# Kernel tuning notes

Hardware: AMD Instinct MI355X
Metric: run time of the kernel (lower is better)

The kernel has to match this reference:

```python
import jax, jax.numpy as jnp
import numpy as np


def setup_inputs() -> dict:
    key = jax.random.key(0)
    ks = jax.random.split(key, 8)
    n_src, n_dst, n_edges = 100000, 50000, 600000
    d_in, d_out = 128, 128
    n_reuse, n_cache = 5000, 8000
    full_dst_len = n_dst + n_reuse

    feat_src = jax.random.normal(ks[0], (n_src, d_in), jnp.float32)
    src = jax.random.randint(ks[1], (n_edges,), 0, n_src)
    dst = jax.random.randint(ks[2], (n_edges,), 0, n_dst)
    # xavier-ish init for the two bias-free Linear layers (stored as [out, in] like torch)
    W_self = jax.random.normal(ks[3], (d_out, d_in), jnp.float32) / np.sqrt(d_in).astype(np.float32)
    W_neigh = jax.random.normal(ks[4], (d_out, d_in), jnp.float32) / np.sqrt(d_in).astype(np.float32)
    # reuse_indices must be unique positions within [0, full_dst_len)
    reuse_indices = jnp.sort(jax.random.permutation(ks[5], full_dst_len)[:n_reuse])
    reuse_embedding = jax.random.normal(ks[6], (n_reuse, d_out), jnp.float32)
    cache_indices = jax.random.randint(ks[7], (n_cache,), 0, full_dst_len)
    return dict(feat_src=feat_src, W_self=W_self, W_neigh=W_neigh,
                reuse_embedding=reuse_embedding, src=src, dst=dst,
                reuse_indices=reuse_indices, cache_indices=cache_indices,
                n_dst=n_dst)


def reference(feat_src, W_self, W_neigh, reuse_embedding, src, dst,
              reuse_indices, cache_indices, n_dst):
    # --- GraphSAGE 'mean' aggregation on a block graph ---
    feat_dst = feat_src[:n_dst]                         # [n_dst, D_in]
    msgs = feat_src[src]                                # [E, D_in] copy_src gather
    ssum = jax.ops.segment_sum(msgs, dst, num_segments=n_dst)          # [n_dst, D_in]
    deg = jax.ops.segment_sum(jnp.ones_like(msgs[:, 0]), dst, num_segments=n_dst)
    h_neigh = jnp.where(deg[:, None] > 0, ssum / jnp.maximum(deg, 1.0)[:, None], 0.0)
    rst = feat_dst @ W_self.T + h_neigh @ W_neigh.T     # fc_self + fc_neigh

    # --- cache-reuse scatter merge (flag == 0 path) ---
    n_reuse = reuse_indices.shape[0]
    full_dst_len = n_dst + n_reuse
    keep = jnp.ones((full_dst_len,), dtype=bool).at[reuse_indices].set(False)
    unprune_indices = jnp.nonzero(keep, size=n_dst)[0]  # np.delete equivalent
    full = jnp.zeros((full_dst_len, rst.shape[1]), rst.dtype)
    full = full.at[unprune_indices].set(rst).at[reuse_indices].set(reuse_embedding)
    cache_embedding = jax.lax.stop_gradient(full[cache_indices])  # .detach()
    return full, cache_embedding
```

## Files before the change

### kernel.cpp

```cpp
#include <hip/hip_runtime.h>

#define N_SRC   100000
#define N_DST   50000
#define D       128
#define MAXDEG  64

#define NB      391
#define CHUNKS  256
#define TOTAL_BLOCKS 2048
#define COUNT_BLOCKS 256

typedef __attribute__((ext_vector_type(8))) short bf16x8;
typedef __attribute__((ext_vector_type(4))) float f32x4;

__device__ __forceinline__ unsigned short f2bf(float f) {
    unsigned u = __float_as_uint(f);
    u += 0x7FFFu + ((u >> 16) & 1u);
    return (unsigned short)(u >> 16);
}
__device__ __forceinline__ float bf2f(unsigned short u) {
    return __uint_as_float((unsigned)u << 16);
}

__global__ __launch_bounds__(256)
void prep_count_kernel(const int* __restrict__ dst,
                       int* __restrict__ cntmatT,
                       int n_edges, int cb,
                       const int* __restrict__ reuse_idx,
                       int* __restrict__ rowpos, int n_reuse,
                       const float* __restrict__ Wself,
                       const float* __restrict__ Wneigh,
                       unsigned short* __restrict__ wbf,
                       const float* __restrict__ feat,
                       unsigned int* __restrict__ featbf_u32) {
    __shared__ int lc[NB];
    if (blockIdx.x < COUNT_BLOCKS) {
        for (int i = threadIdx.x; i < NB; i += 256) lc[i] = 0;
        __syncthreads();
        int c = blockIdx.x;
        int e0 = c * cb, e1 = min(n_edges, e0 + cb);
        for (int e = e0 + (int)threadIdx.x; e < e1; e += 256)
            atomicAdd(&lc[dst[e] >> 7], 1);
        __syncthreads();
        for (int i = threadIdx.x; i < NB; i += 256)
            cntmatT[i * CHUNKS + c] = lc[i];
    } else {
        int stid = (blockIdx.x - COUNT_BLOCKS) * 256 + threadIdx.x;
        const int sstride = (TOTAL_BLOCKS - COUNT_BLOCKS) * 256;

        if (stid < N_DST) {
            int lo = 0, hi = n_reuse;
            while (lo < hi) {
                int mid = (lo + hi) >> 1;
                if (reuse_idx[mid] - mid > stid) hi = mid; else lo = mid + 1;
            }
            rowpos[stid] = stid + lo;
        }
        if (stid < 128 * 256) {
            int n = stid >> 8;
            int k = stid & 255;
            float v = (k < 128) ? Wself[n * 128 + k] : Wneigh[n * 128 + (k - 128)];
            wbf[stid] = f2bf(v);
        }
        const int n4 = N_SRC * (D / 4);
        for (int i = stid; i < n4; i += sstride) {
            float4 v = *(const float4*)(feat + (size_t)i * 4);
            uint2 o;
            o.x = (unsigned)f2bf(v.x) | ((unsigned)f2bf(v.y) << 16);
            o.y = (unsigned)f2bf(v.z) | ((unsigned)f2bf(v.w) << 16);
            *(uint2*)(featbf_u32 + (size_t)i * 2) = o;
        }
    }
}

__global__ __launch_bounds__(256)
void bucket_scan_kernel(const int* __restrict__ cntmatT,
                        int* __restrict__ offrel,
                        int* __restrict__ bsum) {
    __shared__ int s[CHUNKS];
    int k = blockIdx.x;
    int t = threadIdx.x;
    int x = cntmatT[k * CHUNKS + t];
    s[t] = x;
    __syncthreads();
#pragma unroll
    for (int off = 1; off < CHUNKS; off <<= 1) {
        int v = (t >= off) ? s[t - off] : 0;
        __syncthreads();
        s[t] += v;
        __syncthreads();
    }
    offrel[k * CHUNKS + t] = s[t] - x;
    if (t == CHUNKS - 1) bsum[k] = s[t];
}

__global__ __launch_bounds__(256)
void base_scan_kernel(const int* __restrict__ bsum,
                      int* __restrict__ bucketbase) {
    __shared__ int s[NB];
    __shared__ int tot;
    int t = threadIdx.x;
    for (int i = t; i < NB; i += 256) s[i] = bsum[i];
    __syncthreads();
    if (t == 0) {
        int run = 0;
        for (int i = 0; i < NB; ++i) { int v = s[i]; s[i] = run; run += v; }
        tot = run;
    }
    __syncthreads();
    for (int i = t; i < NB; i += 256) bucketbase[i] = s[i];
    if (t == 0) bucketbase[NB] = tot;
}

__global__ __launch_bounds__(256)
void scatter_kernel(const int* __restrict__ src,
                    const int* __restrict__ dst,
                    const int* __restrict__ offrel,
                    const int* __restrict__ bucketbase,
                    uint2* __restrict__ pe,
                    int n_edges, int cb) {
    __shared__ int lc[NB];
    for (int i = threadIdx.x; i < NB; i += 256) lc[i] = 0;
    __syncthreads();
    int c = blockIdx.x;
    int e0 = c * cb, e1 = min(n_edges, e0 + cb);
    for (int e = e0 + (int)threadIdx.x; e < e1; e += 256) {
        int d = dst[e];
        int s = src[e];
        int k = d >> 7;
        int r = atomicAdd(&lc[k], 1);
        int pos = bucketbase[k] + offrel[k * CHUNKS + c] + r;
        pe[pos] = make_uint2((unsigned)s, (unsigned)d);
    }
}

__global__ __launch_bounds__(256)
void fine_ell_kernel(const uint2* __restrict__ pe,
                     const int* __restrict__ bucketbase,
                     int* __restrict__ ell,
                     int* __restrict__ cnt) {
    __shared__ int rc[128];
    int k = blockIdx.x;
    if (threadIdx.x < 128) rc[threadIdx.x] = 0;
    __syncthreads();
    int e0 = bucketbase[k], e1 = bucketbase[k + 1];
    for (int e = e0 + (int)threadIdx.x; e < e1; e += 256) {
        uint2 p = pe[e];
        int d = (int)p.y;
        int slot = atomicAdd(&rc[d & 127], 1);
        if (slot < MAXDEG)
            ell[(size_t)d * MAXDEG + slot] = (int)p.x;
    }
    __syncthreads();
    int row = k * 128 + threadIdx.x;
    if (threadIdx.x < 128 && row < N_DST) cnt[row] = rc[threadIdx.x];
}

__global__ __launch_bounds__(256)
void gather_bf16_kernel(const unsigned short* __restrict__ featbf,
                        const int* __restrict__ ell,
                        const int* __restrict__ cnt,
                        uint4* __restrict__ hneigh_u4) {
    int gid  = blockIdx.x * blockDim.x + threadIdx.x;
    int row  = gid >> 4;
    int lane = gid & 15;
    if (row >= N_DST) return;

    int deg = cnt[row];
    int n = min(deg, MAXDEG);
    float inv = 1.0f / fmaxf((float)deg, 1.0f);
    const int* rell = ell + (size_t)row * MAXDEG;

    float acc[8];
#pragma unroll
    for (int k = 0; k < 8; ++k) acc[k] = 0.f;

    union U { uint4 v; unsigned short us[8]; };
    int j = 0;
    for (; j + 4 <= n; j += 4) {
        int s0 = rell[j + 0];
        int s1 = rell[j + 1];
        int s2 = rell[j + 2];
        int s3 = rell[j + 3];
        U a, b, c, d;
        a.v = *(const uint4*)(featbf + (size_t)s0 * D + lane * 8);
        b.v = *(const uint4*)(featbf + (size_t)s1 * D + lane * 8);
        c.v = *(const uint4*)(featbf + (size_t)s2 * D + lane * 8);
        d.v = *(const uint4*)(featbf + (size_t)s3 * D + lane * 8);
#pragma unroll
        for (int k = 0; k < 8; ++k)
            acc[k] += (bf2f(a.us[k]) + bf2f(b.us[k])) + (bf2f(c.us[k]) + bf2f(d.us[k]));
    }
    for (; j < n; ++j) {
        int s = rell[j];
        U a;
        a.v = *(const uint4*)(featbf + (size_t)s * D + lane * 8);
#pragma unroll
        for (int k = 0; k < 8; ++k) acc[k] += bf2f(a.us[k]);
    }
    uint4 o;
    o.x = (unsigned)f2bf(acc[0] * inv) | ((unsigned)f2bf(acc[1] * inv) << 16);
    o.y = (unsigned)f2bf(acc[2] * inv) | ((unsigned)f2bf(acc[3] * inv) << 16);
    o.z = (unsigned)f2bf(acc[4] * inv) | ((unsigned)f2bf(acc[5] * inv) << 16);
    o.w = (unsigned)f2bf(acc[6] * inv) | ((unsigned)f2bf(acc[7] * inv) << 16);
    hneigh_u4[(size_t)row * 16 + lane] = o;
}

__global__ __launch_bounds__(256, 2)
void gemm_kernel(const unsigned short* __restrict__ featbf,
                 const unsigned short* __restrict__ hneigh,
                 const unsigned short* __restrict__ wbf,
                 const int* __restrict__ rowpos,
                 float* __restrict__ full) {
    __shared__ unsigned short Wl[128 * 256];

    int tid = threadIdx.x;
    {
        int n = tid >> 1;
        int ckbase = (tid & 1) * 16;
        const uint4* s = (const uint4*)(wbf + n * 256);
        uint4* d = (uint4*)(Wl + n * 256);
#pragma unroll
        for (int i = 0; i < 16; ++i) {
            int ck = ckbase + i;
            d[ck ^ (n & 7)] = s[ck];
        }
    }
    __syncthreads();

    int wv   = tid >> 6;
    int lane = tid & 63;
    int l15  = lane & 15;
    int q    = lane >> 4;
    int rowbase = blockIdx.x * 128 + wv * 32;

    f32x4 acc[2][8];
#pragma unroll
    for (int rt = 0; rt < 2; ++rt)
#pragma unroll
        for (int ct = 0; ct < 8; ++ct) acc[rt][ct] = (f32x4){0.f, 0.f, 0.f, 0.f};

    int r0c = min(rowbase + l15,      N_DST - 1);
    int r1c = min(rowbase + 16 + l15, N_DST - 1);

#pragma unroll
    for (int s = 0; s < 8; ++s) {
        const unsigned short* A = (s < 4) ? featbf : hneigh;
        int k0 = (s & 3) * 32 + q * 8;
        bf16x8 a0 = *(const bf16x8*)(A + (size_t)r0c * D + k0);
        bf16x8 a1 = *(const bf16x8*)(A + (size_t)r1c * D + k0);
#pragma unroll
        for (int ct = 0; ct < 8; ++ct) {
            int n = ct * 16 + l15;
            int ck = s * 4 + q;
            bf16x8 b = *(const bf16x8*)(Wl + n * 256 + ((ck ^ (n & 7)) << 3));
            acc[0][ct] = __builtin_amdgcn_mfma_f32_16x16x32_bf16(a0, b, acc[0][ct], 0, 0, 0);
            acc[1][ct] = __builtin_amdgcn_mfma_f32_16x16x32_bf16(a1, b, acc[1][ct], 0, 0, 0);
        }
    }

#pragma unroll
    for (int rt = 0; rt < 2; ++rt) {
#pragma unroll
        for (int reg = 0; reg < 4; ++reg) {
            int gm = rowbase + rt * 16 + q * 4 + reg;
            if (gm < N_DST) {
                int jj = rowpos[gm];
                float* outr = full + (size_t)jj * D + l15;
#pragma unroll
                for (int ct = 0; ct < 8; ++ct)
                    outr[ct * 16] = acc[rt][ct][reg];
            }
        }
    }
}

__global__ __launch_bounds__(256)
void epilogue_kernel(const float* __restrict__ emb,
                     const int* __restrict__ ridx, int n_reuse,
                     float* __restrict__ full,
                     const int* __restrict__ cidx,
                     float* __restrict__ cache_out, int n_cache) {
    int idx = blockIdx.x * blockDim.x + threadIdx.x;
    int row = idx >> 5;
    int c4 = (idx & 31) * 4;
    if (row < n_reuse) {
        *(float4*)&full[(size_t)ridx[row] * D + c4] =
            *(const float4*)&emb[(size_t)row * D + c4];
    } else if (row < n_reuse + n_cache) {
        int r = row - n_reuse;
        int v = cidx[r];
        int lo = 0, hi = n_reuse;
        while (lo < hi) {
            int mid = (lo + hi) >> 1;
            if (ridx[mid] < v) lo = mid + 1; else hi = mid;
        }
        const float* srcp = (lo < n_reuse && ridx[lo] == v)
            ? emb + (size_t)lo * D
            : full + (size_t)v * D;
        *(float4*)&cache_out[(size_t)r * D + c4] = *(const float4*)&srcp[c4];
    }
}

extern "C" void kernel_launch(void* const* d_in, const int* in_sizes, int n_in,
                              void* d_out, int out_size, void* d_ws, size_t ws_size,
                              hipStream_t stream) {
    const float* feat_src  = (const float*)d_in[0];
    const float* W_self    = (const float*)d_in[1];
    const float* W_neigh   = (const float*)d_in[2];
    const float* reuse_emb = (const float*)d_in[3];
    const int*   src       = (const int*)d_in[4];
    const int*   dst       = (const int*)d_in[5];
    const int*   reuse_idx = (const int*)d_in[6];
    const int*   cache_idx = (const int*)d_in[7];

    int n_edges = in_sizes[4];
    int n_reuse = in_sizes[6];
    int n_cache = in_sizes[7];
    int full_len = N_DST + n_reuse;
    int cb = (n_edges + CHUNKS - 1) / CHUNKS;

    float* full = (float*)d_out;
    float* cache_out = full + (size_t)full_len * D;

    size_t hneigh_b = (size_t)N_DST * D * sizeof(unsigned short);
    size_t featbf_b = (size_t)N_SRC * D * sizeof(unsigned short);

    unsigned short* hneigh = (unsigned short*)d_ws;
    unsigned short* featbf = (unsigned short*)((char*)d_ws + hneigh_b);
    int*   cnt    = (int*)((char*)featbf + featbf_b);
    int*   rowpos = cnt + N_DST;
    unsigned short* wbf = (unsigned short*)(rowpos + N_DST);
    int*   cntmatT = (int*)(wbf + 128 * 256);
    int*   offrel  = cntmatT + NB * CHUNKS;
    int*   bsum    = offrel + NB * CHUNKS;
    int*   bucketbase = bsum + NB;
    uint2* pe = (uint2*)(bucketbase + NB + 2);
    pe = (uint2*)(((size_t)pe + 7) & ~(size_t)7);

    int* ell = (int*)full;

    prep_count_kernel<<<TOTAL_BLOCKS, 256, 0, stream>>>(
        dst, cntmatT, n_edges, cb,
        reuse_idx, rowpos, n_reuse, W_self, W_neigh, wbf,
        feat_src, (unsigned int*)featbf);

    bucket_scan_kernel<<<NB, 256, 0, stream>>>(cntmatT, offrel, bsum);

    base_scan_kernel<<<1, 256, 0, stream>>>(bsum, bucketbase);

    scatter_kernel<<<CHUNKS, 256, 0, stream>>>(
        src, dst, offrel, bucketbase, pe, n_edges, cb);

    fine_ell_kernel<<<NB, 256, 0, stream>>>(pe, bucketbase, ell, cnt);

    gather_bf16_kernel<<<(N_DST * 16 + 255) / 256, 256, 0, stream>>>(
        featbf, ell, cnt, (uint4*)hneigh);

    gemm_kernel<<<(N_DST + 127) / 128, 256, 0, stream>>>(
        featbf, hneigh, wbf, rowpos, full);

    epilogue_kernel<<<((n_reuse + n_cache) * 32 + 255) / 256, 256, 0, stream>>>(
        reuse_emb, reuse_idx, n_reuse, full, cache_idx, cache_out, n_cache);
}
```

Measured before the change: 187.1 us.

## Fuse fine bucketing with neighbor gather using shared-memory ELL per 32-row bucket

Buckets shrink from 128 to 32 destination rows, and the fine ELL build is merged into the gather kernel. Each block now builds its neighbor lists in shared memory and immediately computes the mean aggregation, so the global ELL array and count array are never written and read back. Edge records are packed into 32 bits (source index shifted, row-in-bucket in the low bits), which halves scatter traffic. The bucket-base scan is parallelized to handle the larger bucket count. In exchange, the count and offset matrices are four times larger and per-block shared-memory atomics and LDS footprint go up.

Result: no change. 183.6 us (-1.9%).

```diff
diff --git a/kernel.cpp b/kernel.cpp
--- a/kernel.cpp
+++ b/kernel.cpp
@@ -5,7 +5,8 @@
 #define D       128
 #define MAXDEG  64
 
-#define NB      391
+#define RPB     32
+#define NB      1563
 #define CHUNKS  256
 #define TOTAL_BLOCKS 2048
 #define COUNT_BLOCKS 256
@@ -40,7 +41,7 @@
         int c = blockIdx.x;
         int e0 = c * cb, e1 = min(n_edges, e0 + cb);
         for (int e = e0 + (int)threadIdx.x; e < e1; e += 256)
-            atomicAdd(&lc[dst[e] >> 7], 1);
+            atomicAdd(&lc[dst[e] >> 5], 1);
         __syncthreads();
         for (int i = threadIdx.x; i < NB; i += 256)
             cntmatT[i * CHUNKS + c] = lc[i];
@@ -97,19 +98,34 @@
 __global__ __launch_bounds__(256)
 void base_scan_kernel(const int* __restrict__ bsum,
                       int* __restrict__ bucketbase) {
-    __shared__ int s[NB];
-    __shared__ int tot;
+    const int PER = (NB + 255) / 256;
+    __shared__ int part[256];
     int t = threadIdx.x;
-    for (int i = t; i < NB; i += 256) s[i] = bsum[i];
-    __syncthreads();
-    if (t == 0) {
-        int run = 0;
-        for (int i = 0; i < NB; ++i) { int v = s[i]; s[i] = run; run += v; }
-        tot = run;
-    }
-    __syncthreads();
-    for (int i = t; i < NB; i += 256) bucketbase[i] = s[i];
-    if (t == 0) bucketbase[NB] = tot;
+    int local[PER];
+    int run = 0;
+#pragma unroll
+    for (int i = 0; i < PER; ++i) {
+        int idx = t * PER + i;
+        int v = (idx < NB) ? bsum[idx] : 0;
+        local[i] = run;
+        run += v;
+    }
+    part[t] = run;
+    __syncthreads();
+#pragma unroll
+    for (int off = 1; off < 256; off <<= 1) {
+        int v = (t >= off) ? part[t - off] : 0;
+        __syncthreads();
+        part[t] += v;
+        __syncthreads();
+    }
+    int segbase = part[t] - run;
+#pragma unroll
+    for (int i = 0; i < PER; ++i) {
+        int idx = t * PER + i;
+        if (idx < NB) bucketbase[idx] = segbase + local[i];
+    }
+    if (t == 255) bucketbase[NB] = part[255];
 }
 
 __global__ __launch_bounds__(256)
@@ -117,7 +133,7 @@
                     const int* __restrict__ dst,
                     const int* __restrict__ offrel,
                     const int* __restrict__ bucketbase,
-                    uint2* __restrict__ pe,
+                    unsigned int* __restrict__ pe,
                     int n_edges, int cb) {
     __shared__ int lc[NB];
     for (int i = threadIdx.x; i < NB; i += 256) lc[i] = 0;
@@ -127,83 +143,80 @@
     for (int e = e0 + (int)threadIdx.x; e < e1; e += 256) {
         int d = dst[e];
         int s = src[e];
-        int k = d >> 7;
+        int k = d >> 5;
         int r = atomicAdd(&lc[k], 1);
         int pos = bucketbase[k] + offrel[k * CHUNKS + c] + r;
-        pe[pos] = make_uint2((unsigned)s, (unsigned)d);
-    }
-}
-
-__global__ __launch_bounds__(256)
-void fine_ell_kernel(const uint2* __restrict__ pe,
-                     const int* __restrict__ bucketbase,
-                     int* __restrict__ ell,
-                     int* __restrict__ cnt) {
-    __shared__ int rc[128];
+        pe[pos] = ((unsigned)s << 5) | (unsigned)(d & 31);
+    }
+}
+
+__global__ __launch_bounds__(256)
+void fine_gather_kernel(const unsigned int* __restrict__ pe,
+                        const int* __restrict__ bucketbase,
+                        const unsigned short* __restrict__ featbf,
+                        uint4* __restrict__ hneigh_u4) {
+    __shared__ int lell[RPB * MAXDEG];
+    __shared__ int rc[RPB];
     int k = blockIdx.x;
-    if (threadIdx.x < 128) rc[threadIdx.x] = 0;
+    int tid = threadIdx.x;
+    if (tid < RPB) rc[tid] = 0;
     __syncthreads();
     int e0 = bucketbase[k], e1 = bucketbase[k + 1];
-    for (int e = e0 + (int)threadIdx.x; e < e1; e += 256) {
-        uint2 p = pe[e];
-        int d = (int)p.y;
-        int slot = atomicAdd(&rc[d & 127], 1);
+    for (int e = e0 + tid; e < e1; e += 256) {
+        unsigned p = pe[e];
+        int rl = (int)(p & 31u);
+        int slot = atomicAdd(&rc[rl], 1);
         if (slot < MAXDEG)
-            ell[(size_t)d * MAXDEG + slot] = (int)p.x;
-    }
-    __syncthreads();
-    int row = k * 128 + threadIdx.x;
-    if (threadIdx.x < 128 && row < N_DST) cnt[row] = rc[threadIdx.x];
-}
-
-__global__ __launch_bounds__(256)
-void gather_bf16_kernel(const unsigned short* __restrict__ featbf,
-                        const int* __restrict__ ell,
-                        const int* __restrict__ cnt,
-                        uint4* __restrict__ hneigh_u4) {
-    int gid  = blockIdx.x * blockDim.x + threadIdx.x;
-    int row  = gid >> 4;
-    int lane = gid & 15;
-    if (row >= N_DST) return;
-
-    int deg = cnt[row];
-    int n = min(deg, MAXDEG);
-    float inv = 1.0f / fmaxf((float)deg, 1.0f);
-    const int* rell = ell + (size_t)row * MAXDEG;
-
-    float acc[8];
-#pragma unroll
-    for (int k = 0; k < 8; ++k) acc[k] = 0.f;
+            lell[rl * MAXDEG + slot] = (int)(p >> 5);
+    }
+    __syncthreads();
 
     union U { uint4 v; unsigned short us[8]; };
-    int j = 0;
-    for (; j + 4 <= n; j += 4) {
-        int s0 = rell[j + 0];
-        int s1 = rell[j + 1];
-        int s2 = rell[j + 2];
-        int s3 = rell[j + 3];
-        U a, b, c, d;
-        a.v = *(const uint4*)(featbf + (size_t)s0 * D + lane * 8);
-        b.v = *(const uint4*)(featbf + (size_t)s1 * D + lane * 8);
-        c.v = *(const uint4*)(featbf + (size_t)s2 * D + lane * 8);
-        d.v = *(const uint4*)(featbf + (size_t)s3 * D + lane * 8);
-#pragma unroll
-        for (int k = 0; k < 8; ++k)
-            acc[k] += (bf2f(a.us[k]) + bf2f(b.us[k])) + (bf2f(c.us[k]) + bf2f(d.us[k]));
-    }
-    for (; j < n; ++j) {
-        int s = rell[j];
-        U a;
-        a.v = *(const uint4*)(featbf + (size_t)s * D + lane * 8);
-#pragma unroll
-        for (int k = 0; k < 8; ++k) acc[k] += bf2f(a.us[k]);
-    }
-    uint4 o;
-    o.x = (unsigned)f2bf(acc[0] * inv) | ((unsigned)f2bf(acc[1] * inv) << 16);
-    o.y = (unsigned)f2bf(acc[2] * inv) | ((unsigned)f2bf(acc[3] * inv) << 16);
-    o.z = (unsigned)f2bf(acc[4] * inv) | ((unsigned)f2bf(acc[5] * inv) << 16);
-    o.w = (unsigned)f2bf(acc[6] * inv) | ((unsigned)f2bf(acc[7] * inv) << 16);
-    hneigh_u4[(size_t)row * 16 + lane] = o;
+#pragma unroll
+    for (int pass = 0; pass < 2; ++pass) {
+        int rl   = pass * 16 + (tid >> 4);
+        int lane = tid & 15;
+        int row  = k * RPB + rl;
+        if (row < N_DST) {
+            int deg = rc[rl];
+            int n = min(deg, MAXDEG);
+            float inv = 1.0f / fmaxf((float)deg, 1.0f);
+            const int* lst = lell + rl * MAXDEG;
+
+            float acc[8];
+#pragma unroll
+            for (int q = 0; q < 8; ++q) acc[q] = 0.f;
+
+            int j = 0;
+            for (; j + 4 <= n; j += 4) {
+                int s0 = lst[j + 0];
+                int s1 = lst[j + 1];
+                int s2 = lst[j + 2];
+                int s3 = lst[j + 3];
+                U a, b, c, d;
+                a.v = *(const uint4*)(featbf + (size_t)s0 * D + lane * 8);
+                b.v = *(const uint4*)(featbf + (size_t)s1 * D + lane * 8);
+                c.v = *(const uint4*)(featbf + (size_t)s2 * D + lane * 8);
+                d.v = *(const uint4*)(featbf + (size_t)s3 * D + lane * 8);
+#pragma unroll
+                for (int q = 0; q < 8; ++q)
+                    acc[q] += (bf2f(a.us[q]) + bf2f(b.us[q])) + (bf2f(c.us[q]) + bf2f(d.us[q]));
+            }
+            for (; j < n; ++j) {
+                int s = lst[j];
+                U a;
+                a.v = *(const uint4*)(featbf + (size_t)s * D + lane * 8);
+#pragma unroll
+                for (int q = 0; q < 8; ++q) acc[q] += bf2f(a.us[q]);
+            }
+            uint4 o;
+            o.x = (unsigned)f2bf(acc[0] * inv) | ((unsigned)f2bf(acc[1] * inv) << 16);
+            o.y = (unsigned)f2bf(acc[2] * inv) | ((unsigned)f2bf(acc[3] * inv) << 16);
+            o.z = (unsigned)f2bf(acc[4] * inv) | ((unsigned)f2bf(acc[5] * inv) << 16);
+            o.w = (unsigned)f2bf(acc[6] * inv) | ((unsigned)f2bf(acc[7] * inv) << 16);
+            hneigh_u4[(size_t)row * 16 + lane] = o;
+        }
+    }
 }
 
 __global__ __launch_bounds__(256, 2)
@@ -328,17 +341,13 @@
 
     unsigned short* hneigh = (unsigned short*)d_ws;
     unsigned short* featbf = (unsigned short*)((char*)d_ws + hneigh_b);
-    int*   cnt    = (int*)((char*)featbf + featbf_b);
-    int*   rowpos = cnt + N_DST;
+    int*   rowpos = (int*)((char*)featbf + featbf_b);
     unsigned short* wbf = (unsigned short*)(rowpos + N_DST);
     int*   cntmatT = (int*)(wbf + 128 * 256);
-    int*   offrel  = cntmatT + NB * CHUNKS;
-    int*   bsum    = offrel + NB * CHUNKS;
+    int*   offrel  = cntmatT + (size_t)NB * CHUNKS;
+    int*   bsum    = offrel + (size_t)NB * CHUNKS;
     int*   bucketbase = bsum + NB;
-    uint2* pe = (uint2*)(bucketbase + NB + 2);
-    pe = (uint2*)(((size_t)pe + 7) & ~(size_t)7);
-
-    int* ell = (int*)full;
+    unsigned int* pe = (unsigned int*)(bucketbase + NB + 1);
 
     prep_count_kernel<<<TOTAL_BLOCKS, 256, 0, stream>>>(
         dst, cntmatT, n_edges, cb,
@@ -352,10 +361,8 @@
     scatter_kernel<<<CHUNKS, 256, 0, stream>>>(
         src, dst, offrel, bucketbase, pe, n_edges, cb);
 
-    fine_ell_kernel<<<NB, 256, 0, stream>>>(pe, bucketbase, ell, cnt);
-
-    gather_bf16_kernel<<<(N_DST * 16 + 255) / 256, 256, 0, stream>>>(
-        featbf, ell, cnt, (uint4*)hneigh);
+    fine_gather_kernel<<<NB, 256, 0, stream>>>(
+        pe, bucketbase, featbf, (uint4*)hneigh);
 
     gemm_kernel<<<(N_DST + 127) / 128, 256, 0, stream>>>(
         featbf, hneigh, wbf, rowpos, full);
```
